# Kernel tuning notes

Hardware: AMD Instinct MI355X
Metric: run time of the kernel (lower is better)

The kernel has to match this reference:

```python
import jax, jax.numpy as jnp
import numpy as np

NG, NR, C = 50000, 12000, 128     # lane nodes, roi nodes, n_map
NS = 6                            # num_scales
EPS, ELR, E1, E2 = 50000, 5000, 150000, 150000
GN_EPS = 1e-5


def gn(x, sb):
    # GroupNorm(num_groups=1) on [N, C]: normalize over C per row (biased var)
    m = x.mean(-1, keepdims=True)
    v = x.var(-1, keepdims=True)
    return (x - m) / jnp.sqrt(v + GN_EPS) * sb[0] + sb[1]


def lane_pooling(ctx_feat, ctx_pose, tgt_feat, tgt_pose, hi, wi,
                 input_w, relpose_w, relpose_b, ctx1_w, ctx1_gn, ctx2_w,
                 mlp1_w, mlp1_gn, mlp2_w, mlp2_gn, norm_gn):
    dist_feat = jax.nn.relu((ctx_pose[hi] - tgt_pose[wi]) @ relpose_w.T + relpose_b)  # [E,128]
    ctx = jnp.concatenate([ctx_feat[hi], dist_feat], -1)                               # [E,256]
    ctx = jax.nn.relu(gn(ctx @ ctx1_w.T, ctx1_gn)) @ ctx2_w.T                          # [E,128]
    identity = tgt_feat
    t = tgt_feat @ input_w.T
    t = t.at[wi].add(ctx)                 # scatter-reduce onto target nodes
    t = jax.nn.relu(gn(t, norm_gn))
    t = jax.nn.relu(gn(t @ mlp1_w.T, mlp1_gn))
    t = gn(t @ mlp2_w.T, mlp2_gn)
    return jax.nn.relu(t + identity)


def global_graph(feat, ps_u, ps_v, lr_u, lr_v,
                 ctr_w, ps_w, left_w, right_w, norm_gn, ctr2_w, ctr2_gn):
    res = feat
    for i in range(4):  # 4 fusion layers (structurally distinct weights)
        temp = feat @ ctr_w[i].T
        for k in range(2 * NS):  # pre0..pre5, suc0..suc5
            temp = temp.at[ps_u[k]].add(feat[ps_v[k]] @ ps_w[i, k].T)
        temp = temp.at[lr_u[0]].add(feat[lr_v[0]] @ left_w[i].T)
        temp = temp.at[lr_u[1]].add(feat[lr_v[1]] @ right_w[i].T)
        feat = jax.nn.relu(gn(temp, norm_gn[i]))
        feat = gn(feat @ ctr2_w[i].T, ctr2_gn[i])
        feat = jax.nn.relu(feat + res)
        res = feat
    return feat


def _gn_pack(key, lead):
    k1, k2 = jax.random.split(key)
    scale = 1.0 + 0.1 * jax.random.normal(k1, lead + (C,), jnp.float32)
    bias = 0.1 * jax.random.normal(k2, lead + (C,), jnp.float32)
    return jnp.stack([scale, bias], axis=-2)  # [..., 2, C]


def setup_inputs() -> dict:
    key = jax.random.key(0)
    ks = jax.random.split(key, 32)
    w = lambda k, sh: 0.05 * jax.random.normal(k, sh, jnp.float32)
    inp = {
        'roi_feat': jax.random.normal(ks[0], (NR, C), jnp.float32),
        'graph_pose': jax.random.normal(ks[1], (NG, 4), jnp.float32),
        'roi_pose': jax.random.normal(ks[2], (NR, 4), jnp.float32),
        'lp_input_w': w(ks[3], (2, C, C)),
        'lp_relpose_w': w(ks[4], (2, C, 4)),
        'lp_relpose_b': w(ks[5], (2, C)),
        'lp_ctx1_w': w(ks[6], (2, C, 2 * C)),
        'lp_ctx1_gn': _gn_pack(ks[7], (2,)),
        'lp_ctx2_w': w(ks[8], (2, C, C)),
        'lp_mlp1_w': w(ks[9], (2, C, C)),
        'lp_mlp1_gn': _gn_pack(ks[10], (2,)),
        'lp_mlp2_w': w(ks[11], (2, C, C)),
        'lp_mlp2_gn': _gn_pack(ks[12], (2,)),
        'lp_norm_gn': _gn_pack(ks[13], (2,)),
        'fuse_ctr_w': w(ks[14], (4, C, C)),
        'fuse_ps_w': w(ks[15], (4, 2 * NS, C, C)),
        'fuse_left_w': w(ks[16], (4, C, C)),
        'fuse_right_w': w(ks[17], (4, C, C)),
        'fuse_norm_gn': _gn_pack(ks[18], (4,)),
        'fuse_ctr2_w': w(ks[19], (4, C, C)),
        'fuse_ctr2_gn': _gn_pack(ks[20], (4,)),
        'e1_hi': jax.random.randint(ks[21], (E1,), 0, NR, jnp.int32),
        'e1_wi': jax.random.randint(ks[22], (E1,), 0, NG, jnp.int32),
        'e2_hi': jax.random.randint(ks[23], (E2,), 0, NG, jnp.int32),
        'e2_wi': jax.random.randint(ks[24], (E2,), 0, NR, jnp.int32),
        'ps_u': jax.random.randint(ks[25], (2 * NS, EPS), 0, NG, jnp.int32),
        'ps_v': jax.random.randint(ks[26], (2 * NS, EPS), 0, NG, jnp.int32),
        'lr_u': jax.random.randint(ks[27], (2, ELR), 0, NG, jnp.int32),
        'lr_v': jax.random.randint(ks[28], (2, ELR), 0, NG, jnp.int32),
    }
    return inp


def reference(roi_feat, graph_pose, roi_pose, lp_input_w, lp_relpose_w, lp_relpose_b,
              lp_ctx1_w, lp_ctx1_gn, lp_ctx2_w, lp_mlp1_w, lp_mlp1_gn, lp_mlp2_w,
              lp_mlp2_gn, lp_norm_gn, fuse_ctr_w, fuse_ps_w, fuse_left_w, fuse_right_w,
              fuse_norm_gn, fuse_ctr2_w, fuse_ctr2_gn, e1_hi, e1_wi, e2_hi, e2_wi,
              ps_u, ps_v, lr_u, lr_v):
    lp = lambda j: (lp_input_w[j], lp_relpose_w[j], lp_relpose_b[j], lp_ctx1_w[j],
                    lp_ctx1_gn[j], lp_ctx2_w[j], lp_mlp1_w[j], lp_mlp1_gn[j],
                    lp_mlp2_w[j], lp_mlp2_gn[j], lp_norm_gn[j])
    graph_feat = jnp.zeros((NG, C), jnp.float32)
    # roi2graph: context = roi, target = graph
    graph_feat = lane_pooling(roi_feat, roi_pose, graph_feat, graph_pose, e1_hi, e1_wi, *lp(0))
    graph_feat = global_graph(graph_feat, ps_u, ps_v, lr_u, lr_v,
                              fuse_ctr_w, fuse_ps_w, fuse_left_w, fuse_right_w,
                              fuse_norm_gn, fuse_ctr2_w, fuse_ctr2_gn)
    # graph2roi: context = graph, target = roi
    out = lane_pooling(graph_feat, graph_pose, roi_feat, roi_pose, e2_hi, e2_wi, *lp(1))
    return out
```

## Files before the change

### kernel.cpp

```cpp
#include <hip/hip_runtime.h>

#define NG 50000
#define NR 12000
#define EPS_N 50000
#define ELR_N 5000
#define E1_N 150000
#define E2_N 150000
#define GN_EPS_F 1e-5f
#define SCAN_CHUNK 4096
#define WST 136
#define SST 176

typedef __attribute__((ext_vector_type(8))) __bf16 bf16x8;
typedef __attribute__((ext_vector_type(4))) float f32x4;
typedef __attribute__((ext_vector_type(2))) float f32x2;

__device__ __forceinline__ bf16x8 cvt8(const float* __restrict__ p) {
    float4 x0 = *reinterpret_cast<const float4*>(p);
    float4 x1 = *reinterpret_cast<const float4*>(p + 4);
    bf16x8 a;
    a[0] = (__bf16)x0.x; a[1] = (__bf16)x0.y; a[2] = (__bf16)x0.z; a[3] = (__bf16)x0.w;
    a[4] = (__bf16)x1.x; a[5] = (__bf16)x1.y; a[6] = (__bf16)x1.z; a[7] = (__bf16)x1.w;
    return a;
}

__device__ __forceinline__ unsigned f32_to_fp8(float f) {
    f = fminf(f, 448.f);
    unsigned bits = __float_as_uint(f);
    int e = (int)((bits >> 23) & 0xff) - 127;
    if (e < -9) return 0u;
    if (e < -6) {
        return (unsigned)(int)(f * 512.f + 0.5f);
    }
    unsigned m = (bits >> 20) & 7;
    unsigned r = (bits >> 19) & 1;
    unsigned em = ((unsigned)(e + 7) << 3) | m;
    em += r;
    if (em > 0x7Eu) em = 0x7Eu;
    return em;
}

struct PrepTab { const float* src[80]; int stride[80]; int n; };

__global__ void prepw_k(PrepTab tab, __bf16* __restrict__ wbuf)
{
    int t = blockIdx.x * 256 + threadIdx.x;
    int w = t >> 11;
    if (w >= tab.n) return;
    int rr = t & 2047;
    int chunk = rr >> 6, l = rr & 63;
    int wn = chunk >> 4, ks = (chunk >> 2) & 3, ni = chunk & 3;
    int c = wn * 64 + ni * 16 + (l & 15);
    int kb = (ks * 4 + (l >> 4)) * 8;
    const float* s = tab.src[w] + (size_t)c * tab.stride[w] + kb;
    bf16x8 o;
    #pragma unroll
    for (int e = 0; e < 8; ++e) o[e] = (__bf16)s[e];
    *reinterpret_cast<bf16x8*>(wbuf + (size_t)w * 16384 + rr * 8) = o;
}

__global__ void hist14_k(const int* __restrict__ ps_u, const int* __restrict__ lr_u,
                         int* __restrict__ cnt)
{
    int t = blockIdx.x * 256 + threadIdx.x;
    const int total = 12 * EPS_N + 2 * ELR_N;
    if (t >= total) return;
    int k, u;
    if (t < 12 * EPS_N) { k = t / EPS_N; u = ps_u[t]; }
    else { int r = t - 12 * EPS_N; k = 12 + r / ELR_N; u = lr_u[r]; }
    atomicAdd(&cnt[k * NG + u], 1);
}

__global__ void fill14_k(const int* __restrict__ ps_u, const int* __restrict__ ps_v,
                         const int* __restrict__ lr_u, const int* __restrict__ lr_v,
                         int* __restrict__ head, int* __restrict__ col)
{
    int t = blockIdx.x * 256 + threadIdx.x;
    const int total = 12 * EPS_N + 2 * ELR_N;
    if (t >= total) return;
    int k, u, v;
    if (t < 12 * EPS_N) { k = t / EPS_N; u = ps_u[t]; v = ps_v[t]; }
    else { int r = t - 12 * EPS_N; k = 12 + r / ELR_N; u = lr_u[r]; v = lr_v[r]; }
    int pos = atomicAdd(&head[k * NG + u], 1);
    col[pos] = v;
}

__global__ void histE_k(const int* __restrict__ wi, int n, int* __restrict__ cnt)
{
    int t = blockIdx.x * 256 + threadIdx.x;
    if (t >= n) return;
    atomicAdd(&cnt[wi[t]], 1);
}

__global__ void fillE_k(const int* __restrict__ wi, int n,
                        int* __restrict__ head, int* __restrict__ col)
{
    int t = blockIdx.x * 256 + threadIdx.x;
    if (t >= n) return;
    int pos = atomicAdd(&head[wi[t]], 1);
    col[pos] = t;
}

__global__ void scan1_k(const int* __restrict__ in, int n, int* __restrict__ bsum)
{
    __shared__ int sm[4];
    int base = blockIdx.x * SCAN_CHUNK;
    int s = 0;
    for (int i = threadIdx.x; i < SCAN_CHUNK; i += 256) {
        int idx = base + i;
        s += (idx < n) ? in[idx] : 0;
    }
    #pragma unroll
    for (int off = 1; off < 64; off <<= 1) s += __shfl_xor(s, off);
    if ((threadIdx.x & 63) == 0) sm[threadIdx.x >> 6] = s;
    __syncthreads();
    if (threadIdx.x == 0) bsum[blockIdx.x] = sm[0] + sm[1] + sm[2] + sm[3];
}

__global__ void scan2_k(int* __restrict__ bsum, int nb)
{
    if (threadIdx.x == 0) {
        int acc = 0;
        for (int i = 0; i < nb; ++i) { int t = bsum[i]; bsum[i] = acc; acc += t; }
    }
}

__global__ void scan3_k(const int* __restrict__ in, int n,
                        const int* __restrict__ bsum, int* __restrict__ outp)
{
    __shared__ int sm[256];
    int base = blockIdx.x * SCAN_CHUNK;
    int loc[16]; int s = 0;
    #pragma unroll
    for (int i = 0; i < 16; ++i) {
        int idx = base + threadIdx.x * 16 + i;
        loc[i] = (idx < n) ? in[idx] : 0; s += loc[i];
    }
    sm[threadIdx.x] = s; __syncthreads();
    for (int off = 1; off < 256; off <<= 1) {
        int v = (threadIdx.x >= off) ? sm[threadIdx.x - off] : 0;
        __syncthreads();
        sm[threadIdx.x] += v;
        __syncthreads();
    }
    int tp = (threadIdx.x ? sm[threadIdx.x - 1] : 0) + bsum[blockIdx.x];
    #pragma unroll
    for (int i = 0; i < 16; ++i) {
        int idx = base + threadIdx.x * 16 + i;
        if (idx < n) outp[idx] = tp;
        tp += loc[i];
        if (idx == n - 1) outp[n] = tp;
    }
}

__device__ __forceinline__ void mfma16(f32x4 (&acc)[8], const bf16x8 (&a)[4],
                                       const __bf16* __restrict__ gw, int lane)
{
    const __bf16* gwb = gw + lane * 8;
    #pragma unroll
    for (int ks = 0; ks < 4; ++ks) {
        #pragma unroll
        for (int n2 = 0; n2 < 8; ++n2) {
            const int chunk = (n2 >> 2) * 16 + ks * 4 + (n2 & 3);
            bf16x8 b = *reinterpret_cast<const bf16x8*>(gwb + chunk * 512);
            acc[n2] = __builtin_amdgcn_mfma_f32_16x16x32_bf16(a[ks], b, acc[n2], 0, 0, 0);
        }
    }
}

__device__ __forceinline__ void ss_to_frags(const float (&ss)[32], bf16x8 (&a)[4])
{
    #pragma unroll
    for (int ks = 0; ks < 4; ++ks)
        #pragma unroll
        for (int i = 0; i < 8; ++i)
            a[ks][i] = (__bf16)ss[ks * 8 + i];
}

__device__ __forceinline__ void gn_mi(const f32x4 (&acc)[8], float (&m)[4], float (&inv)[4])
{
    #pragma unroll
    for (int reg = 0; reg < 4; ++reg) {
        float s = 0.f, q = 0.f;
        #pragma unroll
        for (int n2 = 0; n2 < 8; ++n2) { float v = acc[n2][reg]; s += v; q = fmaf(v, v, q); }
        #pragma unroll
        for (int off = 1; off < 16; off <<= 1) {
            s += __shfl_xor(s, off);
            q += __shfl_xor(q, off);
        }
        m[reg] = s * (1.f / 128.f);
        inv[reg] = rsqrtf(fmaxf(q * (1.f / 128.f) - m[reg] * m[reg], 0.f) + GN_EPS_F);
    }
}

__device__ __forceinline__ void gn_relayout(const f32x4 (&acc)[8], const float* __restrict__ sb,
                                            __bf16* wl, bf16x8 (&a)[4], int r16, int kq)
{
    float m[4], inv[4];
    gn_mi(acc, m, inv);
    #pragma unroll
    for (int reg = 0; reg < 4; ++reg) {
        #pragma unroll
        for (int n2 = 0; n2 < 8; ++n2) {
            const int colc = n2 * 16 + r16;
            float y = (acc[n2][reg] - m[reg]) * inv[reg] * sb[colc] + sb[128 + colc];
            wl[(kq * 4 + reg) * WST + colc] = (__bf16)fmaxf(y, 0.f);
        }
    }
    #pragma unroll
    for (int ks = 0; ks < 4; ++ks)
        a[ks] = *reinterpret_cast<const bf16x8*>(wl + r16 * WST + ks * 32 + kq * 8);
}

template<typename CT>
__launch_bounds__(128, 3)
__global__ void edgefull_k(const int* __restrict__ hi_idx, const int* __restrict__ wi_idx,
                           const CT* __restrict__ ctxfeat,
                           const float* __restrict__ cpose, const float* __restrict__ tpose,
                           const float* __restrict__ rpw, const float* __restrict__ rpb,
                           const __bf16* __restrict__ wc1A, const __bf16* __restrict__ wc1B,
                           const float* __restrict__ sb,
                           __bf16* __restrict__ hout, int M)
{
    __shared__ float rw[640];
    const int tid = threadIdx.x, lane = tid & 63, wv = tid >> 6;
    const int r16 = lane & 15, kq = lane >> 4;
    const int wbase = blockIdx.x * 32 + wv * 16;
    const int erow = wbase + r16;
    const int ec = erow < M ? erow : M - 1;

    for (int i = tid; i < 640; i += 128)
        rw[i] = (i < 512) ? rpw[i] : rpb[i - 512];
    __syncthreads();

    const int hi = hi_idx[ec], wi = wi_idx[ec];
    float4 cp = *reinterpret_cast<const float4*>(cpose + (size_t)hi * 4);
    float4 tp = *reinterpret_cast<const float4*>(tpose + (size_t)wi * 4);
    const float d0 = cp.x - tp.x, d1 = cp.y - tp.y, d2 = cp.z - tp.z, d3 = cp.w - tp.w;

    f32x4 acc[8];
    #pragma unroll
    for (int n2 = 0; n2 < 8; ++n2) acc[n2] = (f32x4){0.f, 0.f, 0.f, 0.f};

    {
        bf16x8 a[4];
        const CT* sp = ctxfeat + (size_t)hi * 128 + kq * 8;
        #pragma unroll
        for (int ks = 0; ks < 4; ++ks) {
            if constexpr (sizeof(CT) == 4) a[ks] = cvt8((const float*)sp + ks * 32);
            else a[ks] = *reinterpret_cast<const bf16x8*>((const __bf16*)sp + ks * 32);
        }
        mfma16(acc, a, wc1A, lane);
    }
    {
        bf16x8 a[4];
        #pragma unroll
        for (int ks = 0; ks < 4; ++ks)
            #pragma unroll
            for (int i = 0; i < 8; ++i) {
                const int k = ks * 32 + kq * 8 + i;
                float4 w4 = *reinterpret_cast<const float4*>(&rw[k * 4]);
                float d = fmaf(d0, w4.x, fmaf(d1, w4.y, fmaf(d2, w4.z,
                          fmaf(d3, w4.w, rw[512 + k]))));
                a[ks][i] = (__bf16)fmaxf(d, 0.f);
            }
        mfma16(acc, a, wc1B, lane);
    }

    float m[4], inv[4];
    gn_mi(acc, m, inv);
    #pragma unroll
    for (int reg = 0; reg < 4; ++reg) {
        const int crow = wbase + kq * 4 + reg;
        if (crow < M) {
            __bf16* dp = hout + (size_t)crow * 128 + r16;
            #pragma unroll
            for (int n2 = 0; n2 < 8; ++n2) {
                const int colc = n2 * 16 + r16;
                float y = (acc[n2][reg] - m[reg]) * inv[reg] * sb[colc] + sb[128 + colc];
                dp[n2 * 16] = (__bf16)fmaxf(y, 0.f);
            }
        }
    }
}

struct FW { const __bf16* w[16]; };

__launch_bounds__(128, 3)
__global__ void fusedlayer_k(const __bf16* __restrict__ feat,
                             const unsigned char* __restrict__ feat8,
                             const int* __restrict__ rp, const int* __restrict__ col,
                             FW fw, const float* __restrict__ gn1,
                             const float* __restrict__ gn2,
                             __bf16* __restrict__ outp,
                             unsigned char* __restrict__ out8, int M)
{
    __shared__ __bf16 wl[2][16 * WST];
    __shared__ unsigned char stage[2][16 * SST];
    const int tid = threadIdx.x, lane = tid & 63, wv = tid >> 6;
    const int r16 = lane & 15, kq = lane >> 4;
    const int wbase = blockIdx.x * 32 + wv * 16;
    const int wrow = (wbase + r16) < M ? (wbase + r16) : M - 1;
    unsigned char* st = stage[wv] + r16 * SST;

    f32x4 acc[8];
    #pragma unroll
    for (int n2 = 0; n2 < 8; ++n2) acc[n2] = (f32x4){0.f, 0.f, 0.f, 0.f};

    #pragma unroll
    for (int j = 0; j < 15; ++j) {
        float ss[32];
        if (j == 14) {
            const __bf16* sp = feat + (size_t)wrow * 128 + kq * 8;
            #pragma unroll
            for (int ks = 0; ks < 4; ++ks) {
                bf16x8 h = *reinterpret_cast<const bf16x8*>(sp + ks * 32);
                #pragma unroll
                for (int i = 0; i < 8; ++i) ss[ks * 8 + i] = (float)h[i];
            }
        } else {
            #pragma unroll
            for (int i = 0; i < 32; ++i) ss[i] = 0.f;
            const int b = rp[j * M + wrow], e = rp[j * M + wrow + 1];
            for (int t2 = b; t2 < e; ++t2) {
                const unsigned char* sp = feat8 + (size_t)col[t2] * 128;
                uint4 q0 = *reinterpret_cast<const uint4*>(sp + kq * 16);
                uint4 q1 = *reinterpret_cast<const uint4*>(sp + 64 + kq * 16);
                *reinterpret_cast<uint4*>(st + kq * 16) = q0;
                *reinterpret_cast<uint4*>(st + 64 + kq * 16) = q1;
                #pragma unroll
                for (int ks = 0; ks < 4; ++ks) {
                    uint2 u = *reinterpret_cast<const uint2*>(st + ks * 32 + kq * 8);
                    f32x2 v0 = __builtin_amdgcn_cvt_pk_f32_fp8(u.x, false);
                    f32x2 v1 = __builtin_amdgcn_cvt_pk_f32_fp8(u.x, true);
                    f32x2 v2 = __builtin_amdgcn_cvt_pk_f32_fp8(u.y, false);
                    f32x2 v3 = __builtin_amdgcn_cvt_pk_f32_fp8(u.y, true);
                    ss[ks*8+0] += v0[0]; ss[ks*8+1] += v0[1];
                    ss[ks*8+2] += v1[0]; ss[ks*8+3] += v1[1];
                    ss[ks*8+4] += v2[0]; ss[ks*8+5] += v2[1];
                    ss[ks*8+6] += v3[0]; ss[ks*8+7] += v3[1];
                }
            }
        }
        bf16x8 a[4];
        ss_to_frags(ss, a);
        mfma16(acc, a, fw.w[j], lane);
    }

    bf16x8 a2[4];
    gn_relayout(acc, gn1, wl[wv], a2, r16, kq);
    f32x4 acc2[8];
    #pragma unroll
    for (int n2 = 0; n2 < 8; ++n2) acc2[n2] = (f32x4){0.f, 0.f, 0.f, 0.f};
    mfma16(acc2, a2, fw.w[15], lane);

    float m[4], inv[4];
    gn_mi(acc2, m, inv);
    #pragma unroll
    for (int reg = 0; reg < 4; ++reg) {
        const int crow = wbase + kq * 4 + reg;
        if (crow < M) {
            __bf16* dp = outp + (size_t)crow * 128 + r16;
            unsigned char* d8 = out8 + (size_t)crow * 128 + r16;
            const __bf16* rs = feat + (size_t)crow * 128 + r16;
            #pragma unroll
            for (int n2 = 0; n2 < 8; ++n2) {
                const int colc = n2 * 16 + r16;
                float y = (acc2[n2][reg] - m[reg]) * inv[reg] * gn2[colc] + gn2[128 + colc];
                y += (float)rs[n2 * 16];
                y = fmaxf(y, 0.f);
                dp[n2 * 16] = (__bf16)y;
                d8[n2 * 16] = (unsigned char)f32_to_fp8(y);
            }
        }
    }
}

template<bool LP2>
__launch_bounds__(128, 3)
__global__ void lptail_k(const __bf16* __restrict__ hsrc,
                         const int* __restrict__ rp, const int* __restrict__ col,
                         const float* __restrict__ roi,
                         const __bf16* __restrict__ wc2, const __bf16* __restrict__ winW,
                         const __bf16* __restrict__ wm1, const __bf16* __restrict__ wm2,
                         const float* __restrict__ ngn, const float* __restrict__ m1gn,
                         const float* __restrict__ m2gn,
                         void* __restrict__ outp,
                         unsigned char* __restrict__ out8, int M)
{
    __shared__ __bf16 wl[2][16 * WST];
    const int tid = threadIdx.x, lane = tid & 63, wv = tid >> 6;
    const int r16 = lane & 15, kq = lane >> 4;
    const int wbase = blockIdx.x * 32 + wv * 16;
    const int wrow = (wbase + r16) < M ? (wbase + r16) : M - 1;

    f32x4 acc[8];
    #pragma unroll
    for (int n2 = 0; n2 < 8; ++n2) acc[n2] = (f32x4){0.f, 0.f, 0.f, 0.f};

    {
        float ss[32];
        #pragma unroll
        for (int i = 0; i < 32; ++i) ss[i] = 0.f;
        const int b = rp[wrow], e = rp[wrow + 1];
        for (int t2 = b; t2 < e; ++t2) {
            const __bf16* sp = hsrc + (size_t)col[t2] * 128 + kq * 8;
            #pragma unroll
            for (int ks = 0; ks < 4; ++ks) {
                bf16x8 h = *reinterpret_cast<const bf16x8*>(sp + ks * 32);
                #pragma unroll
                for (int i = 0; i < 8; ++i) ss[ks * 8 + i] += (float)h[i];
            }
        }
        bf16x8 a[4];
        ss_to_frags(ss, a);
        mfma16(acc, a, wc2, lane);
    }
    if (LP2) {
        bf16x8 a[4];
        const float* sp = roi + (size_t)wrow * 128 + kq * 8;
        #pragma unroll
        for (int ks = 0; ks < 4; ++ks) a[ks] = cvt8(sp + ks * 32);
        mfma16(acc, a, winW, lane);
    }

    {
        bf16x8 a[4];
        gn_relayout(acc, ngn, wl[wv], a, r16, kq);
        #pragma unroll
        for (int n2 = 0; n2 < 8; ++n2) acc[n2] = (f32x4){0.f, 0.f, 0.f, 0.f};
        mfma16(acc, a, wm1, lane);
    }
    {
        bf16x8 a[4];
        gn_relayout(acc, m1gn, wl[wv], a, r16, kq);
        #pragma unroll
        for (int n2 = 0; n2 < 8; ++n2) acc[n2] = (f32x4){0.f, 0.f, 0.f, 0.f};
        mfma16(acc, a, wm2, lane);
    }

    float m[4], inv[4];
    gn_mi(acc, m, inv);
    #pragma unroll
    for (int reg = 0; reg < 4; ++reg) {
        const int crow = wbase + kq * 4 + reg;
        if (crow < M) {
            #pragma unroll
            for (int n2 = 0; n2 < 8; ++n2) {
                const int colc = n2 * 16 + r16;
                float y = (acc[n2][reg] - m[reg]) * inv[reg] * m2gn[colc] + m2gn[128 + colc];
                if (LP2) {
                    y += roi[(size_t)crow * 128 + colc];
                    ((float*)outp)[(size_t)crow * 128 + colc] = fmaxf(y, 0.f);
                } else {
                    y = fmaxf(y, 0.f);
                    ((__bf16*)outp)[(size_t)crow * 128 + colc] = (__bf16)y;
                    out8[(size_t)crow * 128 + colc] = (unsigned char)f32_to_fp8(y);
                }
            }
        }
    }
}

extern "C" void kernel_launch(void* const* d_in, const int* in_sizes, int n_in,
                              void* d_out, int out_size, void* d_ws, size_t ws_size,
                              hipStream_t stream)
{
    const float* roi_feat   = (const float*)d_in[0];
    const float* graph_pose = (const float*)d_in[1];
    const float* roi_pose   = (const float*)d_in[2];
    const float* lp_input_w = (const float*)d_in[3];
    const float* lp_rpw     = (const float*)d_in[4];
    const float* lp_rpb     = (const float*)d_in[5];
    const float* lp_c1w     = (const float*)d_in[6];
    const float* lp_c1gn    = (const float*)d_in[7];
    const float* lp_c2w     = (const float*)d_in[8];
    const float* lp_m1w     = (const float*)d_in[9];
    const float* lp_m1gn    = (const float*)d_in[10];
    const float* lp_m2w     = (const float*)d_in[11];
    const float* lp_m2gn    = (const float*)d_in[12];
    const float* lp_ngn     = (const float*)d_in[13];
    const float* f_ctrw     = (const float*)d_in[14];
    const float* f_psw      = (const float*)d_in[15];
    const float* f_lw       = (const float*)d_in[16];
    const float* f_rw       = (const float*)d_in[17];
    const float* f_ngn      = (const float*)d_in[18];
    const float* f_c2w      = (const float*)d_in[19];
    const float* f_c2gn     = (const float*)d_in[20];
    const int* e1_hi = (const int*)d_in[21];
    const int* e1_wi = (const int*)d_in[22];
    const int* e2_hi = (const int*)d_in[23];
    const int* e2_wi = (const int*)d_in[24];
    const int* ps_u  = (const int*)d_in[25];
    const int* ps_v  = (const int*)d_in[26];
    const int* lr_u  = (const int*)d_in[27];
    const int* lr_v  = (const int*)d_in[28];
    float* out = (float*)d_out;

    __bf16* gA   = (__bf16*)d_ws;
    __bf16* gB   = gA + (size_t)NG * 128;
    __bf16* hbuf = gB + (size_t)NG * 128;
    __bf16* wbuf = hbuf + (size_t)E1_N * 128;
    unsigned char* g8A = (unsigned char*)(wbuf + (size_t)80 * 16384);
    unsigned char* g8B = g8A + (size_t)NG * 128;
    int* ip      = (int*)(g8B + (size_t)NG * 128);
    int* cnt14   = ip;             ip += 14 * NG;
    int* rp14    = ip;             ip += 14 * NG + 1;
    int* col14   = ip;             ip += 12 * EPS_N + 2 * ELR_N;
    int* cntE1   = ip;             ip += NG;
    int* rpE1    = ip;             ip += NG + 1;
    int* colE1   = ip;             ip += E1_N;
    int* cntE2   = ip;             ip += NR;
    int* rpE2    = ip;             ip += NR + 1;
    int* colE2   = ip;             ip += E2_N;
    int* bsum    = ip;             ip += 256;

    dim3 blk(256), blk128(128);
    const dim3 gNG32((NG + 31) / 32), gNR32((NR + 31) / 32), gE32((E1_N + 31) / 32);
    const int NE14 = 12 * EPS_N + 2 * ELR_N;
    const dim3 gH14((NE14 + 255) / 256);

    PrepTab tab; int nw = 0;
    auto addw = [&](const float* p, int s) { tab.src[nw] = p; tab.stride[nw] = s; ++nw; };
    addw(lp_c1w, 256);
    addw(lp_c1w + 128, 256);
    addw(lp_c1w + 32768, 256);
    addw(lp_c1w + 32768 + 128, 256);
    addw(lp_input_w + 16384, 128);
    addw(lp_c2w, 128); addw(lp_c2w + 16384, 128);
    addw(lp_m1w, 128); addw(lp_m1w + 16384, 128);
    addw(lp_m2w, 128); addw(lp_m2w + 16384, 128);
    for (int i = 0; i < 4; ++i) addw(f_ctrw + (size_t)i * 16384, 128);
    for (int i = 0; i < 4; ++i)
        for (int k = 0; k < 12; ++k) addw(f_psw + ((size_t)i * 12 + k) * 16384, 128);
    for (int i = 0; i < 4; ++i) addw(f_lw + (size_t)i * 16384, 128);
    for (int i = 0; i < 4; ++i) addw(f_rw + (size_t)i * 16384, 128);
    for (int i = 0; i < 4; ++i) addw(f_c2w + (size_t)i * 16384, 128);
    tab.n = nw;
    auto wb = [&](int idx) { return (const __bf16*)(wbuf + (size_t)idx * 16384); };
    prepw_k<<<dim3((nw * 2048 + 255) / 256), blk, 0, stream>>>(tab, wbuf);

    hipMemsetAsync(cnt14, 0, (size_t)14 * NG * 4, stream);
    hist14_k<<<gH14, blk, 0, stream>>>(ps_u, lr_u, cnt14);
    {
        int n = 14 * NG, nb = (n + SCAN_CHUNK - 1) / SCAN_CHUNK;
        scan1_k<<<nb, blk, 0, stream>>>(cnt14, n, bsum);
        scan2_k<<<1, blk, 0, stream>>>(bsum, nb);
        scan3_k<<<nb, blk, 0, stream>>>(cnt14, n, bsum, rp14);
    }
    hipMemcpyAsync(cnt14, rp14, (size_t)14 * NG * 4, hipMemcpyDeviceToDevice, stream);
    fill14_k<<<gH14, blk, 0, stream>>>(ps_u, ps_v, lr_u, lr_v, cnt14, col14);

    hipMemsetAsync(cntE1, 0, (size_t)NG * 4, stream);
    histE_k<<<(E1_N + 255) / 256, blk, 0, stream>>>(e1_wi, E1_N, cntE1);
    {
        int n = NG, nb = (n + SCAN_CHUNK - 1) / SCAN_CHUNK;
        scan1_k<<<nb, blk, 0, stream>>>(cntE1, n, bsum);
        scan2_k<<<1, blk, 0, stream>>>(bsum, nb);
        scan3_k<<<nb, blk, 0, stream>>>(cntE1, n, bsum, rpE1);
    }
    hipMemcpyAsync(cntE1, rpE1, (size_t)NG * 4, hipMemcpyDeviceToDevice, stream);
    fillE_k<<<(E1_N + 255) / 256, blk, 0, stream>>>(e1_wi, E1_N, cntE1, colE1);

    hipMemsetAsync(cntE2, 0, (size_t)NR * 4, stream);
    histE_k<<<(E2_N + 255) / 256, blk, 0, stream>>>(e2_wi, E2_N, cntE2);
    {
        int n = NR, nb = (n + SCAN_CHUNK - 1) / SCAN_CHUNK;
        scan1_k<<<nb, blk, 0, stream>>>(cntE2, n, bsum);
        scan2_k<<<1, blk, 0, stream>>>(bsum, nb);
        scan3_k<<<nb, blk, 0, stream>>>(cntE2, n, bsum, rpE2);
    }
    hipMemcpyAsync(cntE2, rpE2, (size_t)NR * 4, hipMemcpyDeviceToDevice, stream);
    fillE_k<<<(E2_N + 255) / 256, blk, 0, stream>>>(e2_wi, E2_N, cntE2, colE2);

    edgefull_k<float><<<gE32, blk128, 0, stream>>>(
        e1_hi, e1_wi, roi_feat, roi_pose, graph_pose, lp_rpw, lp_rpb,
        wb(0), wb(1), lp_c1gn, hbuf, E1_N);
    lptail_k<false><<<gNG32, blk128, 0, stream>>>(
        hbuf, rpE1, colE1, nullptr, wb(5), nullptr, wb(7), wb(9),
        lp_ngn, lp_m1gn, lp_m2gn, gA, g8A, NG);

    for (int i = 0; i < 4; ++i) {
        FW fw;
        for (int k = 0; k < 12; ++k) fw.w[k] = wb(15 + i * 12 + k);
        fw.w[12] = wb(63 + i); fw.w[13] = wb(67 + i);
        fw.w[14] = wb(11 + i); fw.w[15] = wb(71 + i);
        const __bf16* src = (i & 1) ? gB : gA;
        __bf16* dst = (i & 1) ? gA : gB;
        const unsigned char* src8 = (i & 1) ? g8B : g8A;
        unsigned char* dst8 = (i & 1) ? g8A : g8B;
        fusedlayer_k<<<gNG32, blk128, 0, stream>>>(
            src, src8, rp14, col14, fw, f_ngn + (size_t)i * 256,
            f_c2gn + (size_t)i * 256, dst, dst8, NG);
    }

    edgefull_k<__bf16><<<gE32, blk128, 0, stream>>>(
        e2_hi, e2_wi, gA, graph_pose, roi_pose, lp_rpw + 512, lp_rpb + 128,
        wb(2), wb(3), lp_c1gn + 256, hbuf, E2_N);
    lptail_k<true><<<gNR32, blk128, 0, stream>>>(
        hbuf, rpE2, colE2, roi_feat, wb(6), wb(4), wb(8), wb(10),
        lp_ngn + 256, lp_m1gn + 256, lp_m2gn + 256, out, nullptr, NR);
}
```

Before: 699.4 us.

## Merge all CSR builds into one histogram/scan/fill pass and double-buffer gather staging

Concatenates the fusion-layer adjacency, E1 and E2 edge lists into a single key space. One histogram, one scan and one fill then build every CSR structure, replacing three separate chains of memset, hist, scan, memcpy and fill launches. The aim is to cut launch count and the serialized small-kernel overhead. The fused layer also double-buffers its per-wave LDS staging buffer across neighbor iterations, so consecutive gathers do not reuse the same slot, at the cost of twice the staging shared memory.

```diff
diff --git a/kernel.cpp b/kernel.cpp
--- a/kernel.cpp
+++ b/kernel.cpp
@@ -11,6 +11,11 @@
 #define WST 136
 #define SST 176
 
+#define NKEY (14 * NG + NG + NR)
+#define NEDGE (12 * EPS_N + 2 * ELR_N + E1_N + E2_N)
+#define E1OFF (12 * EPS_N + 2 * ELR_N)
+#define E2OFF (E1OFF + E1_N)
+
 typedef __attribute__((ext_vector_type(8))) __bf16 bf16x8;
 typedef __attribute__((ext_vector_type(4))) float f32x4;
 typedef __attribute__((ext_vector_type(2))) float f32x2;
@@ -29,9 +34,7 @@
     unsigned bits = __float_as_uint(f);
     int e = (int)((bits >> 23) & 0xff) - 127;
     if (e < -9) return 0u;
-    if (e < -6) {
-        return (unsigned)(int)(f * 512.f + 0.5f);
-    }
+    if (e < -6) return (unsigned)(int)(f * 512.f + 0.5f);
     unsigned m = (bits >> 20) & 7;
     unsigned r = (bits >> 19) & 1;
     unsigned em = ((unsigned)(e + 7) << 3) | m;
@@ -59,46 +62,38 @@
     *reinterpret_cast<bf16x8*>(wbuf + (size_t)w * 16384 + rr * 8) = o;
 }
 
-__global__ void hist14_k(const int* __restrict__ ps_u, const int* __restrict__ lr_u,
-                         int* __restrict__ cnt)
+__device__ __forceinline__ int edge_key(int t, const int* ps_u, const int* lr_u,
+                                        const int* e1_wi, const int* e2_wi)
+{
+    if (t < 12 * EPS_N) return (t / EPS_N) * NG + ps_u[t];
+    if (t < E1OFF) { int r = t - 12 * EPS_N; return (12 + r / ELR_N) * NG + lr_u[r]; }
+    if (t < E2OFF) return 14 * NG + e1_wi[t - E1OFF];
+    return 14 * NG + NG + e2_wi[t - E2OFF];
+}
+
+__global__ void histA_k(const int* __restrict__ ps_u, const int* __restrict__ lr_u,
+                        const int* __restrict__ e1_wi, const int* __restrict__ e2_wi,
+                        int* __restrict__ cnt)
 {
     int t = blockIdx.x * 256 + threadIdx.x;
-    const int total = 12 * EPS_N + 2 * ELR_N;
-    if (t >= total) return;
-    int k, u;
-    if (t < 12 * EPS_N) { k = t / EPS_N; u = ps_u[t]; }
-    else { int r = t - 12 * EPS_N; k = 12 + r / ELR_N; u = lr_u[r]; }
-    atomicAdd(&cnt[k * NG + u], 1);
-}
-
-__global__ void fill14_k(const int* __restrict__ ps_u, const int* __restrict__ ps_v,
-                         const int* __restrict__ lr_u, const int* __restrict__ lr_v,
-                         int* __restrict__ head, int* __restrict__ col)
+    if (t >= NEDGE) return;
+    atomicAdd(&cnt[edge_key(t, ps_u, lr_u, e1_wi, e2_wi)], 1);
+}
+
+__global__ void fillA_k(const int* __restrict__ ps_u, const int* __restrict__ lr_u,
+                        const int* __restrict__ e1_wi, const int* __restrict__ e2_wi,
+                        const int* __restrict__ ps_v, const int* __restrict__ lr_v,
+                        int* __restrict__ head, int* __restrict__ col)
 {
     int t = blockIdx.x * 256 + threadIdx.x;
-    const int total = 12 * EPS_N + 2 * ELR_N;
-    if (t >= total) return;
-    int k, u, v;
-    if (t < 12 * EPS_N) { k = t / EPS_N; u = ps_u[t]; v = ps_v[t]; }
-    else { int r = t - 12 * EPS_N; k = 12 + r / ELR_N; u = lr_u[r]; v = lr_v[r]; }
-    int pos = atomicAdd(&head[k * NG + u], 1);
-    col[pos] = v;
-}
-
-__global__ void histE_k(const int* __restrict__ wi, int n, int* __restrict__ cnt)
-{
-    int t = blockIdx.x * 256 + threadIdx.x;
-    if (t >= n) return;
-    atomicAdd(&cnt[wi[t]], 1);
-}
-
-__global__ void fillE_k(const int* __restrict__ wi, int n,
-                        int* __restrict__ head, int* __restrict__ col)
-{
-    int t = blockIdx.x * 256 + threadIdx.x;
-    if (t >= n) return;
-    int pos = atomicAdd(&head[wi[t]], 1);
-    col[pos] = t;
+    if (t >= NEDGE) return;
+    int payload;
+    if (t < 12 * EPS_N) payload = ps_v[t];
+    else if (t < E1OFF) payload = lr_v[t - 12 * EPS_N];
+    else if (t < E2OFF) payload = t - E1OFF;
+    else payload = t - E2OFF;
+    int pos = atomicAdd(&head[edge_key(t, ps_u, lr_u, e1_wi, e2_wi)], 1);
+    col[pos] = payload;
 }
 
 __global__ void scan1_k(const int* __restrict__ in, int n, int* __restrict__ bsum)
@@ -297,16 +292,17 @@
                              unsigned char* __restrict__ out8, int M)
 {
     __shared__ __bf16 wl[2][16 * WST];
-    __shared__ unsigned char stage[2][16 * SST];
+    __shared__ unsigned char stage[2][2][16 * SST];
     const int tid = threadIdx.x, lane = tid & 63, wv = tid >> 6;
     const int r16 = lane & 15, kq = lane >> 4;
     const int wbase = blockIdx.x * 32 + wv * 16;
     const int wrow = (wbase + r16) < M ? (wbase + r16) : M - 1;
-    unsigned char* st = stage[wv] + r16 * SST;
 
     f32x4 acc[8];
     #pragma unroll
     for (int n2 = 0; n2 < 8; ++n2) acc[n2] = (f32x4){0.f, 0.f, 0.f, 0.f};
+
+    int sc = 0;
 
     #pragma unroll
     for (int j = 0; j < 15; ++j) {
@@ -324,6 +320,8 @@
             for (int i = 0; i < 32; ++i) ss[i] = 0.f;
             const int b = rp[j * M + wrow], e = rp[j * M + wrow + 1];
             for (int t2 = b; t2 < e; ++t2) {
+                unsigned char* st = stage[wv][sc & 1] + r16 * SST;
+                sc++;
                 const unsigned char* sp = feat8 + (size_t)col[t2] * 128;
                 uint4 q0 = *reinterpret_cast<const uint4*>(sp + kq * 16);
                 uint4 q1 = *reinterpret_cast<const uint4*>(sp + 64 + kq * 16);
@@ -505,21 +503,13 @@
     unsigned char* g8A = (unsigned char*)(wbuf + (size_t)80 * 16384);
     unsigned char* g8B = g8A + (size_t)NG * 128;
     int* ip      = (int*)(g8B + (size_t)NG * 128);
-    int* cnt14   = ip;             ip += 14 * NG;
-    int* rp14    = ip;             ip += 14 * NG + 1;
-    int* col14   = ip;             ip += 12 * EPS_N + 2 * ELR_N;
-    int* cntE1   = ip;             ip += NG;
-    int* rpE1    = ip;             ip += NG + 1;
-    int* colE1   = ip;             ip += E1_N;
-    int* cntE2   = ip;             ip += NR;
-    int* rpE2    = ip;             ip += NR + 1;
-    int* colE2   = ip;             ip += E2_N;
+    int* cntA    = ip;             ip += NKEY;
+    int* rpAll   = ip;             ip += NKEY + 1;
+    int* colAll  = ip;             ip += NEDGE;
     int* bsum    = ip;             ip += 256;
 
     dim3 blk(256), blk128(128);
     const dim3 gNG32((NG + 31) / 32), gNR32((NR + 31) / 32), gE32((E1_N + 31) / 32);
-    const int NE14 = 12 * EPS_N + 2 * ELR_N;
-    const dim3 gH14((NE14 + 255) / 256);
 
     PrepTab tab; int nw = 0;
     auto addw = [&](const float* p, int s) { tab.src[nw] = p; tab.stride[nw] = s; ++nw; };
@@ -541,44 +531,27 @@
     auto wb = [&](int idx) { return (const __bf16*)(wbuf + (size_t)idx * 16384); };
     prepw_k<<<dim3((nw * 2048 + 255) / 256), blk, 0, stream>>>(tab, wbuf);
 
-    hipMemsetAsync(cnt14, 0, (size_t)14 * NG * 4, stream);
-    hist14_k<<<gH14, blk, 0, stream>>>(ps_u, lr_u, cnt14);
+    hipMemsetAsync(cntA, 0, (size_t)NKEY * 4, stream);
+    histA_k<<<dim3((NEDGE + 255) / 256), blk, 0, stream>>>(ps_u, lr_u, e1_wi, e2_wi, cntA);
     {
-        int n = 14 * NG, nb = (n + SCAN_CHUNK - 1) / SCAN_CHUNK;
-        scan1_k<<<nb, blk, 0, stream>>>(cnt14, n, bsum);
+        int n = NKEY, nb = (n + SCAN_CHUNK - 1) / SCAN_CHUNK;
+        scan1_k<<<nb, blk, 0, stream>>>(cntA, n, bsum);
         scan2_k<<<1, blk, 0, stream>>>(bsum, nb);
-        scan3_k<<<nb, blk, 0, stream>>>(cnt14, n, bsum, rp14);
-    }
-    hipMemcpyAsync(cnt14, rp14, (size_t)14 * NG * 4, hipMemcpyDeviceToDevice, stream);
-    fill14_k<<<gH14, blk, 0, stream>>>(ps_u, ps_v, lr_u, lr_v, cnt14, col14);
-
-    hipMemsetAsync(cntE1, 0, (size_t)NG * 4, stream);
-    histE_k<<<(E1_N + 255) / 256, blk, 0, stream>>>(e1_wi, E1_N, cntE1);
-    {
-        int n = NG, nb = (n + SCAN_CHUNK - 1) / SCAN_CHUNK;
-        scan1_k<<<nb, blk, 0, stream>>>(cntE1, n, bsum);
-        scan2_k<<<1, blk, 0, stream>>>(bsum, nb);
-        scan3_k<<<nb, blk, 0, stream>>>(cntE1, n, bsum, rpE1);
-    }
-    hipMemcpyAsync(cntE1, rpE1, (size_t)NG * 4, hipMemcpyDeviceToDevice, stream);
-    fillE_k<<<(E1_N + 255) / 256, blk, 0, stream>>>(e1_wi, E1_N, cntE1, colE1);
-
-    hipMemsetAsync(cntE2, 0, (size_t)NR * 4, stream);
-    histE_k<<<(E2_N + 255) / 256, blk, 0, stream>>>(e2_wi, E2_N, cntE2);
-    {
-        int n = NR, nb = (n + SCAN_CHUNK - 1) / SCAN_CHUNK;
-        scan1_k<<<nb, blk, 0, stream>>>(cntE2, n, bsum);
-        scan2_k<<<1, blk, 0, stream>>>(bsum, nb);
-        scan3_k<<<nb, blk, 0, stream>>>(cntE2, n, bsum, rpE2);
-    }
-    hipMemcpyAsync(cntE2, rpE2, (size_t)NR * 4, hipMemcpyDeviceToDevice, stream);
-    fillE_k<<<(E2_N + 255) / 256, blk, 0, stream>>>(e2_wi, E2_N, cntE2, colE2);
+        scan3_k<<<nb, blk, 0, stream>>>(cntA, n, bsum, rpAll);
+    }
+    hipMemcpyAsync(cntA, rpAll, (size_t)NKEY * 4, hipMemcpyDeviceToDevice, stream);
+    fillA_k<<<dim3((NEDGE + 255) / 256), blk, 0, stream>>>(
+        ps_u, lr_u, e1_wi, e2_wi, ps_v, lr_v, cntA, colAll);
+
+    const int* rp14 = rpAll;
+    const int* rpE1 = rpAll + 14 * NG;
+    const int* rpE2 = rpAll + 14 * NG + NG;
 
     edgefull_k<float><<<gE32, blk128, 0, stream>>>(
         e1_hi, e1_wi, roi_feat, roi_pose, graph_pose, lp_rpw, lp_rpb,
         wb(0), wb(1), lp_c1gn, hbuf, E1_N);
     lptail_k<false><<<gNG32, blk128, 0, stream>>>(
-        hbuf, rpE1, colE1, nullptr, wb(5), nullptr, wb(7), wb(9),
+        hbuf, rpE1, colAll, nullptr, wb(5), nullptr, wb(7), wb(9),
         lp_ngn, lp_m1gn, lp_m2gn, gA, g8A, NG);
 
     for (int i = 0; i < 4; ++i) {
@@ -591,7 +564,7 @@
         const unsigned char* src8 = (i & 1) ? g8B : g8A;
         unsigned char* dst8 = (i & 1) ? g8A : g8B;
         fusedlayer_k<<<gNG32, blk128, 0, stream>>>(
-            src, src8, rp14, col14, fw, f_ngn + (size_t)i * 256,
+            src, src8, rp14, colAll, fw, f_ngn + (size_t)i * 256,
             f_c2gn + (size_t)i * 256, dst, dst8, NG);
     }
 
@@ -599,6 +572,6 @@
         e2_hi, e2_wi, gA, graph_pose, roi_pose, lp_rpw + 512, lp_rpb + 128,
         wb(2), wb(3), lp_c1gn + 256, hbuf, E2_N);
     lptail_k<true><<<gNR32, blk128, 0, stream>>>(
-        hbuf, rpE2, colE2, roi_feat, wb(6), wb(4), wb(8), wb(10),
+        hbuf, rpE2, colAll, roi_feat, wb(6), wb(4), wb(8), wb(10),
         lp_ngn + 256, lp_m1gn + 256, lp_m2gn + 256, out, nullptr, NR);
 }
```

After: 656.4 us. 6.1% less time.
